# Kernel tuning notes

Hardware: AMD Instinct MI355X
Metric: run time of the kernel (lower is better)

Reference implementation:

```python
import jax, jax.numpy as jnp
import numpy as np

T, I, H = 30, 100, 256  # seq_len, input_size, hidden_size (hard-coded in the module)


def setup_inputs() -> dict:
    key = jax.random.key(0)
    ks = jax.random.split(key, 16)
    B = 512
    N = B * 10  # LSTM batch after view(-1, 30, 100)
    w = lambda k, shape: (jax.random.normal(k, shape, dtype=jnp.float32) * 0.05)
    return {
        "x": jax.random.normal(ks[0], (B, 10, T, I), dtype=jnp.float32),
        "h0": jax.random.normal(ks[1], (2, N, H), dtype=jnp.float32),
        "c0": jax.random.normal(ks[2], (2, N, H), dtype=jnp.float32),
        # PyTorch LSTM params, gate order i,f,g,o; forward and backward directions
        "W_ih_f": w(ks[3], (4 * H, I)),
        "W_hh_f": w(ks[4], (4 * H, H)),
        "b_ih_f": w(ks[5], (4 * H,)),
        "b_hh_f": w(ks[6], (4 * H,)),
        "W_ih_b": w(ks[7], (4 * H, I)),
        "W_hh_b": w(ks[8], (4 * H, H)),
        "b_ih_b": w(ks[9], (4 * H,)),
        "b_hh_b": w(ks[10], (4 * H,)),
        # head: Linear(2560,64) -> Dropout(eval: identity) -> Linear(64,5) -> Softmax
        "W1": w(ks[11], (64, 10 * 256)),
        "b1": w(ks[12], (64,)),
        "W2": w(ks[13], (5, 64)),
        "b2": w(ks[14], (5,)),
    }


def _run_dir(xg, h, c, W_hh):
    """Scan an LSTM direction. xg: [T, N, 4H] precomputed input gates. Returns final h."""
    def step(carry, g_x):
        h, c = carry
        g = g_x + h @ W_hh.T
        i, f, gg, o = jnp.split(g, 4, axis=-1)
        c = jax.nn.sigmoid(f) * c + jax.nn.sigmoid(i) * jnp.tanh(gg)
        h = jax.nn.sigmoid(o) * jnp.tanh(c)
        return (h, c), None
    (h, c), _ = jax.lax.scan(step, (h, c), xg)
    return h


def reference(x, h0, c0, W_ih_f, W_hh_f, b_ih_f, b_hh_f,
              W_ih_b, W_hh_b, b_ih_b, b_hh_b, W1, b1, W2, b2):
    B = x.shape[0]
    xr = x.reshape(-1, T, I)              # [N, 30, 100]
    xs = jnp.transpose(xr, (1, 0, 2))     # [T, N, I] time-major
    # precompute input contributions to gates for all timesteps (one big GEMM)
    xg_f = jnp.einsum('tni,gi->tng', xs, W_ih_f) + b_ih_f + b_hh_f
    xg_b = jnp.einsum('tni,gi->tng', xs[::-1], W_ih_b) + b_ih_b + b_hh_b
    hF = _run_dir(xg_f, h0[0], c0[0], W_hh_f)  # fwd hidden at t=T-1 -> output[:, -1, :256]
    hB = _run_dir(xg_b, h0[1], c0[1], W_hh_b)  # bwd hidden at t=0  -> output[:, 0, 256:]
    # output[:, -1, :128] = hF[:, :128]; output[:, 0, -128:] = hB[:, 128:256]
    x_fea = jnp.concatenate(
        [hF[:, :128].reshape(B, 10, 128), hB[:, 128:256].reshape(B, 10, 128)], axis=-1)
    flat = x_fea.reshape(B, -1)           # [B, 2560]
    z = flat @ W1.T + b1                  # Dropout(0.5) is identity in eval
    logits = z @ W2.T + b2
    y_pred = jax.nn.softmax(logits, axis=-1)
    return (y_pred, x_fea)
```

## Files before the change

kernel.cpp:

```cpp
#include <hip/hip_runtime.h>

typedef __bf16 bf16_t;
typedef __bf16 bf16x8 __attribute__((ext_vector_type(8)));
typedef float f32x4 __attribute__((ext_vector_type(4)));
typedef unsigned long long u64;

#define TSEQ 30
#define ISZ  100
#define HSZ  256
#define NB   5120
#define BATCH 512
#define G4   1024
#define TILE 320
#define NBGRP 16
#define CH   10240
#define SLABX (4 * CH)
#define SLABH (8 * CH)

__device__ __forceinline__ float fsig(float x)  { return 1.0f / (1.0f + __expf(-x)); }
__device__ __forceinline__ float ftanh(float x) { return 2.0f / (1.0f + __expf(-2.0f * x)) - 1.0f; }

__global__ void prep_weights(const float* __restrict__ Wih_f, const float* __restrict__ Whh_f,
                             const float* __restrict__ bih_f, const float* __restrict__ bhh_f,
                             const float* __restrict__ Wih_b, const float* __restrict__ Whh_b,
                             const float* __restrict__ bih_b, const float* __restrict__ bhh_b,
                             bf16_t* __restrict__ Wf, float* __restrict__ bias)
{
    int idx = blockIdx.x * 256 + threadIdx.x;
    if (idx >= 2 * G4 * 384) return;
    int d = idx / (G4 * 384);
    int r = (idx / 384) % G4;
    int k = idx % 384;
    int h = r >> 2, gate = r & 3;
    int grow = gate * HSZ + h;
    const float* Wih = d ? Wih_b : Wih_f;
    const float* Whh = d ? Whh_b : Whh_f;
    float v;
    if (k < ISZ)       v = Wih[grow * ISZ + k];
    else if (k < 128)  v = 0.0f;
    else               v = Whh[grow * HSZ + (k - 128)];
    int mf = r >> 4, lr = r & 15;
    int ks = k >> 5, lq = (k >> 3) & 3, e = k & 7;
    size_t o = ((((size_t)d * 64 + mf) * 12 + ks) * 64 + lq * 16 + lr) * 8 + e;
    Wf[o] = (bf16_t)v;
    if (k == 0) {
        const float* bih = d ? bih_b : bih_f;
        const float* bhh = d ? bhh_b : bhh_f;
        bias[d * G4 + r] = bih[grow] + bhh[grow];
    }
}

__global__ void prep_x(const float* __restrict__ x, bf16_t* __restrict__ xBf)
{
    int idx = blockIdx.x * 256 + threadIdx.x;
    if (idx >= NBGRP * TSEQ * SLABX) return;
    int e    = idx & 7;
    int lane = (idx >> 3) & 63;
    int i2   = idx >> 9;
    int nblk = i2 % 20; i2 /= 20;
    int ks   = i2 & 3;  i2 >>= 2;
    int t    = i2 % TSEQ;
    int bgrp = i2 / TSEQ;
    int n = bgrp * TILE + nblk * 16 + (lane & 15);
    int k = ks * 32 + (lane >> 4) * 8 + e;
    float v = (k < ISZ) ? x[(size_t)n * (TSEQ * ISZ) + t * ISZ + k] : 0.0f;
    xBf[idx] = (bf16_t)v;
}

__global__ void prep_state(const float* __restrict__ h0, bf16_t* __restrict__ hA)
{
    int idx = blockIdx.x * 256 + threadIdx.x;
    if (idx >= 2 * NBGRP * SLABH) return;
    int e    = idx & 7;
    int lane = (idx >> 3) & 63;
    int i2   = idx >> 9;
    int nblk = i2 % 20; i2 /= 20;
    int ksh  = i2 & 7;  i2 >>= 3;
    int bgrp = i2 & 15;
    int dir  = i2 >> 4;
    int col = bgrp * TILE + nblk * 16 + (lane & 15);
    int hid = ksh * 32 + (lane >> 4) * 8 + e;
    hA[idx] = (bf16_t)h0[((size_t)dir * NB + col) * HSZ + hid];
}

__global__ void prep_c(const float* __restrict__ c0, float* __restrict__ cws)
{
    int idx = blockIdx.x * 256 + threadIdx.x;
    if (idx >= 256 * 512 * 20) return;
    int m   = idx & 3;
    int nf  = (idx >> 2) % 5;
    int tid = (idx / 20) & 511;
    int bid = idx / (20 * 512);
    int msub = bid >> 5, dir = (bid >> 4) & 1, bgrp = bid & 15;
    int lane = tid & 63, mw = (tid >> 6) >> 2, nw = (tid >> 6) & 3;
    int lr = lane & 15, lq = lane >> 4;
    int col = bgrp * TILE + nw * 80 + nf * 16 + lr;
    int hid = msub * 32 + mw * 16 + m * 4 + lq;
    cws[idx] = c0[((size_t)dir * NB + col) * HSZ + hid];
}

__global__ void prep_w1t(const float* __restrict__ W1, float* __restrict__ W1T)
{
    int idx = blockIdx.x * 256 + threadIdx.x;
    if (idx >= 2560 * 64) return;
    int k = idx / 64, j = idx % 64;
    W1T[k * 64 + j] = W1[j * 2560 + k];
}

template<bool FAST>
__device__ void run_steps(const bf16_t* __restrict__ xBf,
                          bf16_t* __restrict__ hA, bf16_t* __restrict__ hB,
                          bf16_t* __restrict__ hfin,
                          const bf16_t* wL, bf16_t* pkL, unsigned* mybar,
                          f32x4* c4, const float4* bq,
                          int dir, int bgrp, int msub,
                          int tid, int lane, int mw, int nw, int lr, int lq)
{
#pragma unroll 1
    for (int t = 0; t < TSEQ; ++t) {
        const bf16_t* hs = (t & 1) ? hB : hA;
        bf16_t*       hw = (t & 1) ? hA : hB;
        const int tx = dir ? (TSEQ - 1 - t) : t;
        const bf16_t* xsl = xBf + (size_t)(bgrp * TSEQ + tx) * SLABX + nw * 5 * 512 + lane * 8;
        const bf16_t* hsl = hs + (size_t)(dir * NBGRP + bgrp) * SLABH + nw * 5 * 512 + lane * 8;

        f32x4 acc[4][5] = {};
#pragma unroll
        for (int c = 0; c < 4; ++c) {
            bf16x8 b[5];
#pragma unroll
            for (int nf = 0; nf < 5; ++nf)
                b[nf] = *(const bf16x8*)(xsl + (size_t)c * CH + nf * 512);
            bf16x8 a[4];
#pragma unroll
            for (int m = 0; m < 4; ++m)
                a[m] = *(const bf16x8*)(wL + ((mw * 4 + m) * 12 + c) * 512 + lane * 8);
#pragma unroll
            for (int m = 0; m < 4; ++m)
#pragma unroll
                for (int nf = 0; nf < 5; ++nf)
                    acc[m][nf] = __builtin_amdgcn_mfma_f32_16x16x32_bf16(a[m], b[nf], acc[m][nf], 0, 0, 0);
        }
#pragma unroll
        for (int c = 4; c < 12; ++c) {
            bf16x8 b[5];
#pragma unroll
            for (int nf = 0; nf < 5; ++nf) {
                const bf16_t* src = hsl + (size_t)(c - 4) * CH + nf * 512;
                if (FAST) {
                    b[nf] = *(const bf16x8*)src;
                } else {
                    union { u64 q[2]; bf16x8 v; } u;
                    u.q[0] = __hip_atomic_load((const u64*)src,       __ATOMIC_RELAXED, __HIP_MEMORY_SCOPE_AGENT);
                    u.q[1] = __hip_atomic_load((const u64*)(src + 4), __ATOMIC_RELAXED, __HIP_MEMORY_SCOPE_AGENT);
                    b[nf] = u.v;
                }
            }
            bf16x8 a[4];
#pragma unroll
            for (int m = 0; m < 4; ++m)
                a[m] = *(const bf16x8*)(wL + ((mw * 4 + m) * 12 + c) * 512 + lane * 8);
#pragma unroll
            for (int m = 0; m < 4; ++m)
#pragma unroll
                for (int nf = 0; nf < 5; ++nf)
                    acc[m][nf] = __builtin_amdgcn_mfma_f32_16x16x32_bf16(a[m], b[nf], acc[m][nf], 0, 0, 0);
        }

        if (t < TSEQ - 1) {
#pragma unroll
            for (int m = 0; m < 4; ++m) {
                float4 bb = bq[m];
                int hl = mw * 16 + m * 4 + lq;
#pragma unroll
                for (int nf = 0; nf < 5; ++nf) {
                    f32x4 g = acc[m][nf];
                    float gi = fsig(g[0] + bb.x);
                    float gf = fsig(g[1] + bb.y);
                    float gz = ftanh(g[2] + bb.z);
                    float go = fsig(g[3] + bb.w);
                    float cn = gf * c4[nf][m] + gi * gz;
                    c4[nf][m] = cn;
                    pkL[(nw * 5 + nf) * 512 + ((hl >> 3) * 16 + lr) * 8 + (hl & 7)]
                        = (bf16_t)(go * ftanh(cn));
                }
            }
            __syncthreads();
            bf16_t* dstb = hw + (size_t)(dir * NBGRP + bgrp) * SLABH + (size_t)msub * 20 * 512;
            if (FAST) {
                uint4* dst = (uint4*)dstb;
                const uint4* src = (const uint4*)pkL;
                for (int i = tid; i < 1280; i += 512) dst[i] = src[i];
            } else {
                u64* dst = (u64*)dstb;
                const u64* src = (const u64*)pkL;
                for (int i = tid; i < 2560; i += 512)
                    __hip_atomic_store(&dst[i], src[i], __ATOMIC_RELAXED, __HIP_MEMORY_SCOPE_AGENT);
            }
            __syncthreads();
            if (tid == 0) {
                __hip_atomic_fetch_add(mybar, 1u,
                    FAST ? __ATOMIC_RELAXED : __ATOMIC_RELEASE, __HIP_MEMORY_SCOPE_AGENT);
                while (__hip_atomic_fetch_add(mybar, 0u, __ATOMIC_RELAXED, __HIP_MEMORY_SCOPE_AGENT)
                       < 8u * (unsigned)(t + 2))
                    __builtin_amdgcn_s_sleep(1);
            }
            __syncthreads();
            if (FAST)
                asm volatile("buffer_inv sc0" ::: "memory");
        } else {
#pragma unroll
            for (int m = 0; m < 4; ++m) {
                float4 bb = bq[m];
#pragma unroll
                for (int nf = 0; nf < 5; ++nf) {
                    f32x4 g = acc[m][nf];
                    float gi = fsig(g[0] + bb.x);
                    float gf = fsig(g[1] + bb.y);
                    float gz = ftanh(g[2] + bb.z);
                    float go = fsig(g[3] + bb.w);
                    float cn = gf * c4[nf][m] + gi * gz;
                    float hn = go * ftanh(cn);
                    int col = bgrp * TILE + nw * 80 + nf * 16 + lr;
                    int hid = msub * 32 + mw * 16 + m * 4 + lq;
                    hfin[((size_t)dir * NB + col) * HSZ + hid] = (bf16_t)hn;
                }
            }
        }
    }
}

__global__ __launch_bounds__(512, 1)
void lstm_persist(const bf16_t* __restrict__ Wf, const float* __restrict__ bias,
                  const bf16_t* __restrict__ xBf, const float* __restrict__ cws,
                  bf16_t* __restrict__ hA, bf16_t* __restrict__ hB,
                  bf16_t* __restrict__ hfin, unsigned* __restrict__ bar,
                  unsigned* __restrict__ xccA)
{
    __shared__ __align__(16) bf16_t wL[8 * 12 * 512];
    __shared__ __align__(16) bf16_t pkL[CH];
    __shared__ int sFast;

    const int bid  = blockIdx.x;
    const int msub = bid >> 5;
    const int dir  = (bid >> 4) & 1;
    const int bgrp = bid & 15;
    const int tid  = threadIdx.x;
    const int lane = tid & 63;
    const int mw   = (tid >> 6) >> 2;
    const int nw   = (tid >> 6) & 3;
    const int lr   = lane & 15;
    const int lq   = lane >> 4;

    {
        const uint4* wsrc = (const uint4*)(Wf + ((size_t)dir * 64 + msub * 8) * 12 * 512);
        uint4* wdst = (uint4*)wL;
        for (int i = tid; i < 6144; i += 512) wdst[i] = wsrc[i];
    }
    const float* cp = cws + ((size_t)bid * 512 + tid) * 20;
    f32x4 c4[5];
#pragma unroll
    for (int nf = 0; nf < 5; ++nf) c4[nf] = *(const f32x4*)(cp + nf * 4);
    float4 bq[4];
#pragma unroll
    for (int m = 0; m < 4; ++m)
        bq[m] = *(const float4*)(bias + dir * G4 + (msub * 32 + mw * 16 + m * 4 + lq) * 4);

    unsigned* mybar = bar + (dir * NBGRP + bgrp) * 16;

    unsigned xcc;
    asm volatile("s_getreg_b32 %0, hwreg(HW_REG_XCC_ID)" : "=s"(xcc));
    if (tid == 0) {
        __hip_atomic_store(&xccA[bid], xcc, __ATOMIC_RELAXED, __HIP_MEMORY_SCOPE_AGENT);
        __hip_atomic_fetch_add(mybar, 1u, __ATOMIC_RELEASE, __HIP_MEMORY_SCOPE_AGENT);
        while (__hip_atomic_fetch_add(mybar, 0u, __ATOMIC_RELAXED, __HIP_MEMORY_SCOPE_AGENT) < 8u)
            __builtin_amdgcn_s_sleep(1);
        int ok = (xcc < 8u) ? 1 : 0;
        for (int m2 = 0; m2 < 8; ++m2) {
            unsigned v = __hip_atomic_load(&xccA[m2 * 32 + dir * 16 + bgrp],
                                           __ATOMIC_RELAXED, __HIP_MEMORY_SCOPE_AGENT);
            ok &= (v == xcc) ? 1 : 0;
        }
        sFast = ok;
    }
    __syncthreads();

    if (sFast)
        run_steps<true>(xBf, hA, hB, hfin, wL, pkL, mybar, c4, bq,
                        dir, bgrp, msub, tid, lane, mw, nw, lr, lq);
    else
        run_steps<false>(xBf, hA, hB, hfin, wL, pkL, mybar, c4, bq,
                         dir, bgrp, msub, tid, lane, mw, nw, lr, lq);
}

__global__ __launch_bounds__(256)
void head_kernel(const bf16_t* __restrict__ hfin, const float* __restrict__ W1T,
                 const float* __restrict__ b1, const float* __restrict__ W2,
                 const float* __restrict__ b2, float* __restrict__ out)
{
    __shared__ float flat_s[2560];
    __shared__ float partial[4][64];
    __shared__ float zs[64];
    __shared__ float ls[5];
    __shared__ float es[5];
    int b = blockIdx.x, tid = threadIdx.x;
    const bf16_t* hF = hfin;
    const bf16_t* hB = hfin + (size_t)NB * HSZ;
    float* xfea = out + BATCH * 5 + (size_t)b * 2560;

    for (int j = tid; j < 2560; j += 256) {
        int s = j >> 8, c = j & 255;
        int n = b * 10 + s;
        float v = (c < 128) ? (float)hF[(size_t)n * HSZ + c] : (float)hB[(size_t)n * HSZ + c];
        flat_s[j] = v;
        xfea[j] = v;
    }
    __syncthreads();
    int j = tid & 63, q = tid >> 6;
    float sum = 0.0f;
    for (int k = q * 640; k < (q + 1) * 640; ++k) sum += flat_s[k] * W1T[k * 64 + j];
    partial[q][j] = sum;
    __syncthreads();
    if (tid < 64) zs[tid] = partial[0][tid] + partial[1][tid] + partial[2][tid] + partial[3][tid] + b1[tid];
    __syncthreads();
    if (tid < 5) {
        float l = b2[tid];
        for (int k = 0; k < 64; ++k) l += zs[k] * W2[tid * 64 + k];
        ls[tid] = l;
    }
    __syncthreads();
    if (tid < 5) {
        float m = ls[0];
        for (int k = 1; k < 5; ++k) m = fmaxf(m, ls[k]);
        es[tid] = __expf(ls[tid] - m);
    }
    __syncthreads();
    if (tid < 5) {
        float s5 = es[0] + es[1] + es[2] + es[3] + es[4];
        out[b * 5 + tid] = es[tid] / s5;
    }
}

extern "C" void kernel_launch(void* const* d_in, const int* in_sizes, int n_in,
                              void* d_out, int out_size, void* d_ws, size_t ws_size,
                              hipStream_t stream) {
    const float* x     = (const float*)d_in[0];
    const float* h0    = (const float*)d_in[1];
    const float* c0    = (const float*)d_in[2];
    const float* Wih_f = (const float*)d_in[3];
    const float* Whh_f = (const float*)d_in[4];
    const float* bih_f = (const float*)d_in[5];
    const float* bhh_f = (const float*)d_in[6];
    const float* Wih_b = (const float*)d_in[7];
    const float* Whh_b = (const float*)d_in[8];
    const float* bih_b = (const float*)d_in[9];
    const float* bhh_b = (const float*)d_in[10];
    const float* W1    = (const float*)d_in[11];
    const float* b1    = (const float*)d_in[12];
    const float* W2    = (const float*)d_in[13];
    const float* b2    = (const float*)d_in[14];
    float* out = (float*)d_out;

    uintptr_t ws = (uintptr_t)d_ws;
    bf16_t*   Wf   = (bf16_t*)(ws);
    float*    bias = (float*)(ws + 1572864);
    bf16_t*   xBf  = (bf16_t*)(ws + 1581056);
    bf16_t*   hAb  = (bf16_t*)(ws + 40902656);
    bf16_t*   hBb  = (bf16_t*)(ws + 46145536);
    bf16_t*   hfin = (bf16_t*)(ws + 51388416);
    float*    W1T  = (float*)(ws + 56631296);
    float*    cws  = (float*)(ws + 57286656);
    unsigned* bar  = (unsigned*)(ws + 67772416);
    unsigned* xccA = (unsigned*)(ws + 67774464);

    hipMemsetAsync((void*)bar, 0, 4096, stream);

    prep_weights<<<(2 * G4 * 384 + 255) / 256, 256, 0, stream>>>(
        Wih_f, Whh_f, bih_f, bhh_f, Wih_b, Whh_b, bih_b, bhh_b, Wf, bias);
    prep_x<<<(NBGRP * TSEQ * SLABX + 255) / 256, 256, 0, stream>>>(x, xBf);
    prep_state<<<(2 * NBGRP * SLABH + 255) / 256, 256, 0, stream>>>(h0, hAb);
    prep_c<<<(256 * 512 * 20 + 255) / 256, 256, 0, stream>>>(c0, cws);
    prep_w1t<<<(2560 * 64 + 255) / 256, 256, 0, stream>>>(W1, W1T);

    lstm_persist<<<256, 512, 0, stream>>>(Wf, bias, xBf, cws, hAb, hBb, hfin, bar, xccA);
    head_kernel<<<BATCH, 256, 0, stream>>>(hfin, W1T, b1, W2, b2, out);
}
```

Before: 447.2 us.

## Replace per-step group barrier with per-producer flags and wave-level waits

Drops the full 8-block spin barrier at the end of each LSTM timestep. Each block now bumps its own step counter after publishing its hidden-state slice, and each wave waits only for the producer of the chunk it is about to consume. The input-gate MFMAs run before any waiting, and the cache invalidate moves ahead of the recurrent loads. This lets blocks overlap instead of moving in lockstep, at the cost of more flag polling, a larger flag region to memset, and subtler memory-ordering behaviour on the non-fast path.

Result: slower. 467.0 us (+4.4%).

```diff
diff --git a/kernel.cpp b/kernel.cpp
--- a/kernel.cpp
+++ b/kernel.cpp
@@ -107,22 +107,35 @@
     W1T[k * 64 + j] = W1[j * 2560 + k];
 }
 
+__device__ __forceinline__ void wave_wait(unsigned* flag, unsigned tgt)
+{
+    if ((threadIdx.x & 63) == 0) {
+        while (__hip_atomic_fetch_add(flag, 0u, __ATOMIC_RELAXED, __HIP_MEMORY_SCOPE_AGENT) < tgt)
+            __builtin_amdgcn_s_sleep(1);
+    }
+    __builtin_amdgcn_wave_barrier();
+    __builtin_amdgcn_sched_barrier(0);
+}
+
 template<bool FAST>
 __device__ void run_steps(const bf16_t* __restrict__ xBf,
                           bf16_t* __restrict__ hA, bf16_t* __restrict__ hB,
                           bf16_t* __restrict__ hfin,
-                          const bf16_t* wL, bf16_t* pkL, unsigned* mybar,
+                          const bf16_t* wL, bf16_t* pkL, unsigned* flags,
                           f32x4* c4, const float4* bq,
                           int dir, int bgrp, int msub,
                           int tid, int lane, int mw, int nw, int lr, int lq)
 {
+    const unsigned fo = (unsigned)(nw * 5 * 512 + lane * 8);
+    const bf16_t* wp = wL + (mw * 4 * 12) * 512 + lane * 8;
+
 #pragma unroll 1
     for (int t = 0; t < TSEQ; ++t) {
         const bf16_t* hs = (t & 1) ? hB : hA;
         bf16_t*       hw = (t & 1) ? hA : hB;
         const int tx = dir ? (TSEQ - 1 - t) : t;
-        const bf16_t* xsl = xBf + (size_t)(bgrp * TSEQ + tx) * SLABX + nw * 5 * 512 + lane * 8;
-        const bf16_t* hsl = hs + (size_t)(dir * NBGRP + bgrp) * SLABH + nw * 5 * 512 + lane * 8;
+        const bf16_t* xp = xBf + (size_t)(bgrp * TSEQ + tx) * SLABX + fo;
+        const bf16_t* hp = hs + (size_t)(dir * NBGRP + bgrp) * SLABH + fo;
 
         f32x4 acc[4][5] = {};
 #pragma unroll
@@ -130,23 +143,27 @@
             bf16x8 b[5];
 #pragma unroll
             for (int nf = 0; nf < 5; ++nf)
-                b[nf] = *(const bf16x8*)(xsl + (size_t)c * CH + nf * 512);
+                b[nf] = *(const bf16x8*)(xp + nf * 512);
             bf16x8 a[4];
 #pragma unroll
             for (int m = 0; m < 4; ++m)
-                a[m] = *(const bf16x8*)(wL + ((mw * 4 + m) * 12 + c) * 512 + lane * 8);
+                a[m] = *(const bf16x8*)(wp + (m * 12 + c) * 512);
 #pragma unroll
             for (int m = 0; m < 4; ++m)
 #pragma unroll
                 for (int nf = 0; nf < 5; ++nf)
                     acc[m][nf] = __builtin_amdgcn_mfma_f32_16x16x32_bf16(a[m], b[nf], acc[m][nf], 0, 0, 0);
+            xp += CH;
         }
-#pragma unroll
-        for (int c = 4; c < 12; ++c) {
+        if (FAST)
+            asm volatile("buffer_inv sc0" ::: "memory");
+#pragma unroll
+        for (int c = 0; c < 8; ++c) {
+            if (c != msub) wave_wait(flags + c * 16, (unsigned)t);
             bf16x8 b[5];
 #pragma unroll
             for (int nf = 0; nf < 5; ++nf) {
-                const bf16_t* src = hsl + (size_t)(c - 4) * CH + nf * 512;
+                const bf16_t* src = hp + nf * 512;
                 if (FAST) {
                     b[nf] = *(const bf16x8*)src;
                 } else {
@@ -159,12 +176,13 @@
             bf16x8 a[4];
 #pragma unroll
             for (int m = 0; m < 4; ++m)
-                a[m] = *(const bf16x8*)(wL + ((mw * 4 + m) * 12 + c) * 512 + lane * 8);
+                a[m] = *(const bf16x8*)(wp + (m * 12 + c + 4) * 512);
 #pragma unroll
             for (int m = 0; m < 4; ++m)
 #pragma unroll
                 for (int nf = 0; nf < 5; ++nf)
                     acc[m][nf] = __builtin_amdgcn_mfma_f32_16x16x32_bf16(a[m], b[nf], acc[m][nf], 0, 0, 0);
+            hp += CH;
         }
 
         if (t < TSEQ - 1) {
@@ -186,7 +204,7 @@
                 }
             }
             __syncthreads();
-            bf16_t* dstb = hw + (size_t)(dir * NBGRP + bgrp) * SLABH + (size_t)msub * 20 * 512;
+            bf16_t* dstb = hw + (size_t)(dir * NBGRP + bgrp) * SLABH + (size_t)msub * CH;
             if (FAST) {
                 uint4* dst = (uint4*)dstb;
                 const uint4* src = (const uint4*)pkL;
@@ -198,16 +216,9 @@
                     __hip_atomic_store(&dst[i], src[i], __ATOMIC_RELAXED, __HIP_MEMORY_SCOPE_AGENT);
             }
             __syncthreads();
-            if (tid == 0) {
-                __hip_atomic_fetch_add(mybar, 1u,
+            if (tid == 0)
+                __hip_atomic_fetch_add(flags + msub * 16, 1u,
                     FAST ? __ATOMIC_RELAXED : __ATOMIC_RELEASE, __HIP_MEMORY_SCOPE_AGENT);
-                while (__hip_atomic_fetch_add(mybar, 0u, __ATOMIC_RELAXED, __HIP_MEMORY_SCOPE_AGENT)
-                       < 8u * (unsigned)(t + 2))
-                    __builtin_amdgcn_s_sleep(1);
-            }
-            __syncthreads();
-            if (FAST)
-                asm volatile("buffer_inv sc0" ::: "memory");
         } else {
 #pragma unroll
             for (int m = 0; m < 4; ++m) {
@@ -266,14 +277,15 @@
     for (int m = 0; m < 4; ++m)
         bq[m] = *(const float4*)(bias + dir * G4 + (msub * 32 + mw * 16 + m * 4 + lq) * 4);
 
-    unsigned* mybar = bar + (dir * NBGRP + bgrp) * 16;
+    unsigned* flags  = bar + (dir * NBGRP + bgrp) * 128;
+    unsigned* mybarX = bar + 32 * 128 + (dir * NBGRP + bgrp) * 16;
 
     unsigned xcc;
     asm volatile("s_getreg_b32 %0, hwreg(HW_REG_XCC_ID)" : "=s"(xcc));
     if (tid == 0) {
         __hip_atomic_store(&xccA[bid], xcc, __ATOMIC_RELAXED, __HIP_MEMORY_SCOPE_AGENT);
-        __hip_atomic_fetch_add(mybar, 1u, __ATOMIC_RELEASE, __HIP_MEMORY_SCOPE_AGENT);
-        while (__hip_atomic_fetch_add(mybar, 0u, __ATOMIC_RELAXED, __HIP_MEMORY_SCOPE_AGENT) < 8u)
+        __hip_atomic_fetch_add(mybarX, 1u, __ATOMIC_RELEASE, __HIP_MEMORY_SCOPE_AGENT);
+        while (__hip_atomic_fetch_add(mybarX, 0u, __ATOMIC_RELAXED, __HIP_MEMORY_SCOPE_AGENT) < 8u)
             __builtin_amdgcn_s_sleep(1);
         int ok = (xcc < 8u) ? 1 : 0;
         for (int m2 = 0; m2 < 8; ++m2) {
@@ -286,10 +298,10 @@
     __syncthreads();
 
     if (sFast)
-        run_steps<true>(xBf, hA, hB, hfin, wL, pkL, mybar, c4, bq,
+        run_steps<true>(xBf, hA, hB, hfin, wL, pkL, flags, c4, bq,
                         dir, bgrp, msub, tid, lane, mw, nw, lr, lq);
     else
-        run_steps<false>(xBf, hA, hB, hfin, wL, pkL, mybar, c4, bq,
+        run_steps<false>(xBf, hA, hB, hfin, wL, pkL, flags, c4, bq,
                          dir, bgrp, msub, tid, lane, mw, nw, lr, lq);
 }
 
@@ -371,9 +383,9 @@
     float*    W1T  = (float*)(ws + 56631296);
     float*    cws  = (float*)(ws + 57286656);
     unsigned* bar  = (unsigned*)(ws + 67772416);
-    unsigned* xccA = (unsigned*)(ws + 67774464);
-
-    hipMemsetAsync((void*)bar, 0, 4096, stream);
+    unsigned* xccA = (unsigned*)(ws + 67790848);
+
+    hipMemsetAsync((void*)bar, 0, 18432, stream);
 
     prep_weights<<<(2 * G4 * 384 + 255) / 256, 256, 0, stream>>>(
         Wih_f, Whh_f, bih_f, bhh_f, Wih_b, Whh_b, bih_b, bhh_b, Wf, bias);
```

## Split LSTM hidden dimension across twice as many persistent blocks

Applied to the files above, without the earlier changes.

Doubles the persistent LSTM grid from 256 to 512 blocks by halving the hidden-unit slice each block owns (16 instead of 32 hidden units). Each block keeps half the weights in shared memory, half the accumulators and cell state, and writes a half-size packed h slice. The per-group barrier now waits on 16 blocks instead of 8. The aim is to use more CUs and cut per-step MFMA latency, at the price of more blocks in each barrier and twice as many redundant reads of x and h per block.

After: 520.1 us. +16.3%, slower.

```diff
diff --git a/kernel.cpp b/kernel.cpp
--- a/kernel.cpp
+++ b/kernel.cpp
@@ -86,16 +86,19 @@
 __global__ void prep_c(const float* __restrict__ c0, float* __restrict__ cws)
 {
     int idx = blockIdx.x * 256 + threadIdx.x;
-    if (idx >= 256 * 512 * 20) return;
-    int m   = idx & 3;
-    int nf  = (idx >> 2) % 5;
-    int tid = (idx / 20) & 511;
-    int bid = idx / (20 * 512);
-    int msub = bid >> 5, dir = (bid >> 4) & 1, bgrp = bid & 15;
-    int lane = tid & 63, mw = (tid >> 6) >> 2, nw = (tid >> 6) & 3;
+    if (idx >= 512 * 512 * 10) return;
+    int cell = idx % 10;
+    int m  = cell / 5, nf = cell % 5;
+    int tid = (idx / 10) & 511;
+    int bid = idx / (10 * 512);
+    int dir  = bid >> 8;
+    int msub = (bid >> 4) & 15;
+    int bgrp = bid & 15;
+    int wave = tid >> 6, lane = tid & 63;
+    int mw = wave >> 2, nw = wave & 3;
     int lr = lane & 15, lq = lane >> 4;
     int col = bgrp * TILE + nw * 80 + nf * 16 + lr;
-    int hid = msub * 32 + mw * 16 + m * 4 + lq;
+    int hid = msub * 16 + mw * 8 + m * 4 + lq;
     cws[idx] = c0[((size_t)dir * NB + col) * HSZ + hid];
 }
 
@@ -112,31 +115,33 @@
                           bf16_t* __restrict__ hA, bf16_t* __restrict__ hB,
                           bf16_t* __restrict__ hfin,
                           const bf16_t* wL, bf16_t* pkL, unsigned* mybar,
-                          f32x4* c4, const float4* bq,
+                          float* cst, const float4* bq,
                           int dir, int bgrp, int msub,
                           int tid, int lane, int mw, int nw, int lr, int lq)
 {
+    const unsigned fo = (unsigned)(nw * 5 * 512 + lane * 8);
+
 #pragma unroll 1
     for (int t = 0; t < TSEQ; ++t) {
         const bf16_t* hs = (t & 1) ? hB : hA;
         bf16_t*       hw = (t & 1) ? hA : hB;
         const int tx = dir ? (TSEQ - 1 - t) : t;
-        const bf16_t* xsl = xBf + (size_t)(bgrp * TSEQ + tx) * SLABX + nw * 5 * 512 + lane * 8;
-        const bf16_t* hsl = hs + (size_t)(dir * NBGRP + bgrp) * SLABH + nw * 5 * 512 + lane * 8;
-
-        f32x4 acc[4][5] = {};
+        const bf16_t* xsl = xBf + (size_t)(bgrp * TSEQ + tx) * SLABX + fo;
+        const bf16_t* hsl = hs + (size_t)(dir * NBGRP + bgrp) * SLABH + fo;
+
+        f32x4 acc[2][5] = {};
 #pragma unroll
         for (int c = 0; c < 4; ++c) {
             bf16x8 b[5];
 #pragma unroll
             for (int nf = 0; nf < 5; ++nf)
                 b[nf] = *(const bf16x8*)(xsl + (size_t)c * CH + nf * 512);
-            bf16x8 a[4];
-#pragma unroll
-            for (int m = 0; m < 4; ++m)
-                a[m] = *(const bf16x8*)(wL + ((mw * 4 + m) * 12 + c) * 512 + lane * 8);
-#pragma unroll
-            for (int m = 0; m < 4; ++m)
+            bf16x8 a[2];
+#pragma unroll
+            for (int m = 0; m < 2; ++m)
+                a[m] = *(const bf16x8*)(wL + ((mw * 2 + m) * 12 + c) * 512 + lane * 8);
+#pragma unroll
+            for (int m = 0; m < 2; ++m)
 #pragma unroll
                 for (int nf = 0; nf < 5; ++nf)
                     acc[m][nf] = __builtin_amdgcn_mfma_f32_16x16x32_bf16(a[m], b[nf], acc[m][nf], 0, 0, 0);
@@ -156,12 +161,12 @@
                     b[nf] = u.v;
                 }
             }
-            bf16x8 a[4];
-#pragma unroll
-            for (int m = 0; m < 4; ++m)
-                a[m] = *(const bf16x8*)(wL + ((mw * 4 + m) * 12 + c) * 512 + lane * 8);
-#pragma unroll
-            for (int m = 0; m < 4; ++m)
+            bf16x8 a[2];
+#pragma unroll
+            for (int m = 0; m < 2; ++m)
+                a[m] = *(const bf16x8*)(wL + ((mw * 2 + m) * 12 + c) * 512 + lane * 8);
+#pragma unroll
+            for (int m = 0; m < 2; ++m)
 #pragma unroll
                 for (int nf = 0; nf < 5; ++nf)
                     acc[m][nf] = __builtin_amdgcn_mfma_f32_16x16x32_bf16(a[m], b[nf], acc[m][nf], 0, 0, 0);
@@ -169,9 +174,8 @@
 
         if (t < TSEQ - 1) {
 #pragma unroll
-            for (int m = 0; m < 4; ++m) {
+            for (int m = 0; m < 2; ++m) {
                 float4 bb = bq[m];
-                int hl = mw * 16 + m * 4 + lq;
 #pragma unroll
                 for (int nf = 0; nf < 5; ++nf) {
                     f32x4 g = acc[m][nf];
@@ -179,30 +183,35 @@
                     float gf = fsig(g[1] + bb.y);
                     float gz = ftanh(g[2] + bb.z);
                     float go = fsig(g[3] + bb.w);
-                    float cn = gf * c4[nf][m] + gi * gz;
-                    c4[nf][m] = cn;
-                    pkL[(nw * 5 + nf) * 512 + ((hl >> 3) * 16 + lr) * 8 + (hl & 7)]
+                    float cn = gf * cst[m * 5 + nf] + gi * gz;
+                    cst[m * 5 + nf] = cn;
+                    pkL[(nw * 5 + nf) * 256 + (mw * 16 + lr) * 8 + m * 4 + lq]
                         = (bf16_t)(go * ftanh(cn));
                 }
             }
             __syncthreads();
-            bf16_t* dstb = hw + (size_t)(dir * NBGRP + bgrp) * SLABH + (size_t)msub * 20 * 512;
-            if (FAST) {
-                uint4* dst = (uint4*)dstb;
-                const uint4* src = (const uint4*)pkL;
-                for (int i = tid; i < 1280; i += 512) dst[i] = src[i];
-            } else {
-                u64* dst = (u64*)dstb;
-                const u64* src = (const u64*)pkL;
-                for (int i = tid; i < 2560; i += 512)
-                    __hip_atomic_store(&dst[i], src[i], __ATOMIC_RELAXED, __HIP_MEMORY_SCOPE_AGENT);
+            bf16_t* dstb = hw + (size_t)(dir * NBGRP + bgrp) * SLABH;
+            {
+                int i = tid;
+                for (; i < 640; i += 512) {
+                    int seg = i >> 5, off = i & 31;
+                    uint4 v = *(const uint4*)(pkL + i * 8);
+                    size_t eo = (size_t)(msub >> 1) * CH + seg * 512 + (msub & 1) * 256 + off * 8;
+                    if (FAST) {
+                        *(uint4*)(dstb + eo) = v;
+                    } else {
+                        union { uint4 q; u64 w[2]; } cv; cv.q = v;
+                        __hip_atomic_store((u64*)(dstb + eo),     cv.w[0], __ATOMIC_RELAXED, __HIP_MEMORY_SCOPE_AGENT);
+                        __hip_atomic_store((u64*)(dstb + eo + 4), cv.w[1], __ATOMIC_RELAXED, __HIP_MEMORY_SCOPE_AGENT);
+                    }
+                }
             }
             __syncthreads();
             if (tid == 0) {
                 __hip_atomic_fetch_add(mybar, 1u,
                     FAST ? __ATOMIC_RELAXED : __ATOMIC_RELEASE, __HIP_MEMORY_SCOPE_AGENT);
                 while (__hip_atomic_fetch_add(mybar, 0u, __ATOMIC_RELAXED, __HIP_MEMORY_SCOPE_AGENT)
-                       < 8u * (unsigned)(t + 2))
+                       < 16u * (unsigned)(t + 2))
                     __builtin_amdgcn_s_sleep(1);
             }
             __syncthreads();
@@ -210,8 +219,9 @@
                 asm volatile("buffer_inv sc0" ::: "memory");
         } else {
 #pragma unroll
-            for (int m = 0; m < 4; ++m) {
+            for (int m = 0; m < 2; ++m) {
                 float4 bb = bq[m];
+                int hid = msub * 16 + mw * 8 + m * 4 + lq;
 #pragma unroll
                 for (int nf = 0; nf < 5; ++nf) {
                     f32x4 g = acc[m][nf];
@@ -219,10 +229,9 @@
                     float gf = fsig(g[1] + bb.y);
                     float gz = ftanh(g[2] + bb.z);
                     float go = fsig(g[3] + bb.w);
-                    float cn = gf * c4[nf][m] + gi * gz;
+                    float cn = gf * cst[m * 5 + nf] + gi * gz;
                     float hn = go * ftanh(cn);
                     int col = bgrp * TILE + nw * 80 + nf * 16 + lr;
-                    int hid = msub * 32 + mw * 16 + m * 4 + lq;
                     hfin[((size_t)dir * NB + col) * HSZ + hid] = (bf16_t)hn;
                 }
             }
@@ -230,41 +239,45 @@
     }
 }
 
-__global__ __launch_bounds__(512, 1)
+__global__ __launch_bounds__(512, 4)
 void lstm_persist(const bf16_t* __restrict__ Wf, const float* __restrict__ bias,
                   const bf16_t* __restrict__ xBf, const float* __restrict__ cws,
                   bf16_t* __restrict__ hA, bf16_t* __restrict__ hB,
                   bf16_t* __restrict__ hfin, unsigned* __restrict__ bar,
                   unsigned* __restrict__ xccA)
 {
-    __shared__ __align__(16) bf16_t wL[8 * 12 * 512];
-    __shared__ __align__(16) bf16_t pkL[CH];
+    __shared__ __align__(16) bf16_t wL[4 * 12 * 512];
+    __shared__ __align__(16) bf16_t pkL[5120];
     __shared__ int sFast;
 
     const int bid  = blockIdx.x;
-    const int msub = bid >> 5;
-    const int dir  = (bid >> 4) & 1;
+    const int dir  = bid >> 8;
+    const int msub = (bid >> 4) & 15;
     const int bgrp = bid & 15;
     const int tid  = threadIdx.x;
+    const int wave = tid >> 6;
     const int lane = tid & 63;
-    const int mw   = (tid >> 6) >> 2;
-    const int nw   = (tid >> 6) & 3;
+    const int mw   = wave >> 2;
+    const int nw   = wave & 3;
     const int lr   = lane & 15;
     const int lq   = lane >> 4;
 
     {
-        const uint4* wsrc = (const uint4*)(Wf + ((size_t)dir * 64 + msub * 8) * 12 * 512);
+        const uint4* wsrc = (const uint4*)(Wf + ((size_t)dir * 64 + msub * 4) * 12 * 512);
         uint4* wdst = (uint4*)wL;
-        for (int i = tid; i < 6144; i += 512) wdst[i] = wsrc[i];
-    }
-    const float* cp = cws + ((size_t)bid * 512 + tid) * 20;
-    f32x4 c4[5];
-#pragma unroll
-    for (int nf = 0; nf < 5; ++nf) c4[nf] = *(const f32x4*)(cp + nf * 4);
-    float4 bq[4];
-#pragma unroll
-    for (int m = 0; m < 4; ++m)
-        bq[m] = *(const float4*)(bias + dir * G4 + (msub * 32 + mw * 16 + m * 4 + lq) * 4);
+        for (int i = tid; i < 3072; i += 512) wdst[i] = wsrc[i];
+    }
+    const float* cp = cws + ((size_t)bid * 512 + tid) * 10;
+    float cst[10];
+#pragma unroll
+    for (int i = 0; i < 10; i += 2) {
+        float2 v = *(const float2*)(cp + i);
+        cst[i] = v.x; cst[i + 1] = v.y;
+    }
+    float4 bq[2];
+#pragma unroll
+    for (int m = 0; m < 2; ++m)
+        bq[m] = *(const float4*)(bias + dir * G4 + (msub * 16 + mw * 8 + m * 4 + lq) * 4);
 
     unsigned* mybar = bar + (dir * NBGRP + bgrp) * 16;
 
@@ -273,11 +286,11 @@
     if (tid == 0) {
         __hip_atomic_store(&xccA[bid], xcc, __ATOMIC_RELAXED, __HIP_MEMORY_SCOPE_AGENT);
         __hip_atomic_fetch_add(mybar, 1u, __ATOMIC_RELEASE, __HIP_MEMORY_SCOPE_AGENT);
-        while (__hip_atomic_fetch_add(mybar, 0u, __ATOMIC_RELAXED, __HIP_MEMORY_SCOPE_AGENT) < 8u)
+        while (__hip_atomic_fetch_add(mybar, 0u, __ATOMIC_RELAXED, __HIP_MEMORY_SCOPE_AGENT) < 16u)
             __builtin_amdgcn_s_sleep(1);
         int ok = (xcc < 8u) ? 1 : 0;
-        for (int m2 = 0; m2 < 8; ++m2) {
-            unsigned v = __hip_atomic_load(&xccA[m2 * 32 + dir * 16 + bgrp],
+        for (int m2 = 0; m2 < 16; ++m2) {
+            unsigned v = __hip_atomic_load(&xccA[dir * 256 + m2 * 16 + bgrp],
                                            __ATOMIC_RELAXED, __HIP_MEMORY_SCOPE_AGENT);
             ok &= (v == xcc) ? 1 : 0;
         }
@@ -286,10 +299,10 @@
     __syncthreads();
 
     if (sFast)
-        run_steps<true>(xBf, hA, hB, hfin, wL, pkL, mybar, c4, bq,
+        run_steps<true>(xBf, hA, hB, hfin, wL, pkL, mybar, cst, bq,
                         dir, bgrp, msub, tid, lane, mw, nw, lr, lq);
     else
-        run_steps<false>(xBf, hA, hB, hfin, wL, pkL, mybar, c4, bq,
+        run_steps<false>(xBf, hA, hB, hfin, wL, pkL, mybar, cst, bq,
                          dir, bgrp, msub, tid, lane, mw, nw, lr, lq);
 }
 
@@ -379,9 +392,9 @@
         Wih_f, Whh_f, bih_f, bhh_f, Wih_b, Whh_b, bih_b, bhh_b, Wf, bias);
     prep_x<<<(NBGRP * TSEQ * SLABX + 255) / 256, 256, 0, stream>>>(x, xBf);
     prep_state<<<(2 * NBGRP * SLABH + 255) / 256, 256, 0, stream>>>(h0, hAb);
-    prep_c<<<(256 * 512 * 20 + 255) / 256, 256, 0, stream>>>(c0, cws);
+    prep_c<<<(512 * 512 * 10 + 255) / 256, 256, 0, stream>>>(c0, cws);
     prep_w1t<<<(2560 * 64 + 255) / 256, 256, 0, stream>>>(W1, W1T);
 
-    lstm_persist<<<256, 512, 0, stream>>>(Wf, bias, xBf, cws, hAb, hBb, hfin, bar, xccA);
+    lstm_persist<<<512, 512, 0, stream>>>(Wf, bias, xBf, cws, hAb, hBb, hfin, bar, xccA);
     head_kernel<<<BATCH, 256, 0, stream>>>(hfin, W1T, b1, W2, b2, out);
 }
```
